# Optimization experiments

Measured on AMD Instinct MI355X. Metric: run time of the kernel, lower is better.

## Reference

```python
import jax, jax.numpy as jnp
import numpy as np

B = 1 << 20
N_FREQS = 6          # sin+cos -> 3*2*6 = 36 dims for position
N_BINS = 4           # one-blob bins -> 4 dims per scalar
W_SCALE = 0.18       # ~ sqrt(2/64) He init for ReLU


def freq_embed(p):
    # p: [B,3] -> [B, 3*2*N_FREQS] NeRF-style sin/cos frequency encoding
    freqs = (2.0 ** jnp.arange(N_FREQS, dtype=p.dtype)) * jnp.pi  # [F]
    ang = p[:, :, None] * freqs  # [B,3,F]
    return jnp.concatenate([jnp.sin(ang), jnp.cos(ang)], axis=-1).reshape(p.shape[0], -1)


def one_blob_embed(x):
    # x: [B,D] values in [0,1] -> [B, D*N_BINS] Gaussian one-blob encoding
    centers = (jnp.arange(N_BINS, dtype=x.dtype) + 0.5) / N_BINS  # [K]
    sigma = 1.0 / N_BINS
    val = jnp.exp(-0.5 * ((x[:, :, None] - centers) / sigma) ** 2)  # [B,D,K]
    return val.reshape(x.shape[0], -1)


def to_sphe_coords(d):
    # unit direction [B,3] -> normalized (theta, phi) in [0,1]^2
    theta = jnp.arccos(jnp.clip(d[:, 2], -1.0, 1.0)) / jnp.pi
    phi = jnp.arctan2(d[:, 1], d[:, 0]) / (2.0 * jnp.pi) + 0.5
    return jnp.stack([theta, phi], axis=-1)


def setup_inputs() -> dict:
    key = jax.random.key(0)
    ks = jax.random.split(key, 13)
    p = jax.random.normal(ks[0], (B, 3), dtype=jnp.float32)
    wi = jax.random.normal(ks[1], (B, 3), dtype=jnp.float32)
    wi = wi / jnp.linalg.norm(wi, axis=-1, keepdims=True)
    n = jax.random.normal(ks[2], (B, 3), dtype=jnp.float32)
    n = n / jnp.linalg.norm(n, axis=-1, keepdims=True)
    alpha = jax.random.uniform(ks[3], (B, 3), dtype=jnp.float32)
    beta = jax.random.uniform(ks[4], (B, 3), dtype=jnp.float32)
    r = jax.random.uniform(ks[5], (B, 1), dtype=jnp.float32)
    Ws = {}
    for i in range(6):
        Ws[f"W{i}"] = jax.random.normal(ks[6 + i], (64, 64), dtype=jnp.float32) * W_SCALE
    Ws["W6"] = jax.random.normal(ks[12], (3, 64), dtype=jnp.float32) * W_SCALE
    return dict(p=p, wi=wi, n=n, alpha=alpha, beta=beta, r=r, **Ws)


def reference(p, wi, n, alpha, beta, r, W0, W1, W2, W3, W4, W5, W6):
    x = jnp.concatenate([
        freq_embed(p),                               # 36
        one_blob_embed(to_sphe_coords(wi)),          # 8
        one_blob_embed(to_sphe_coords(n)),           # 8
        one_blob_embed(1.0 - jnp.exp(-r)),           # 4
        alpha,                                       # 3
        beta,                                        # 3
        jnp.ones_like(p[:, :2]),                     # 2 (implicit bias)
    ], axis=-1)  # [B,64]
    h = x
    for W in (W0, W1, W2, W3, W4, W5):
        h = jax.nn.relu(h @ W.T)
    out = h @ W6.T  # [B,3]
    return out * (alpha + beta)  # reflectance factorization
```

## Files before the change

### kernel.cpp

```cpp
#include <hip/hip_runtime.h>

typedef __attribute__((ext_vector_type(8))) short short8;
typedef __attribute__((ext_vector_type(4))) float f32x4;

typedef __attribute__((address_space(3))) unsigned short lds_us;
typedef const __attribute__((address_space(1))) unsigned short glb_us;

__device__ __forceinline__ unsigned short f2bf(float x) {
  union { float f; unsigned u; } v; v.f = x;
  unsigned r = v.u + 0x7fffu + ((v.u >> 16) & 1u);
  return (unsigned short)(r >> 16);
}

#if __has_builtin(__builtin_amdgcn_cvt_pk_bf16_f32)
__device__ __forceinline__ unsigned pk2(float a, float b) {
  return __builtin_bit_cast(unsigned, __builtin_amdgcn_cvt_pk_bf16_f32(a, b));
}
#else
__device__ __forceinline__ unsigned pk2(float a, float b) {
  union { float f; unsigned u; } x, y; x.f = a; y.f = b;
  return __builtin_amdgcn_perm(y.u + 0x8000u, x.u + 0x8000u, 0x07060302u);
}
#endif

__device__ __forceinline__ short8 u2s8(uint4 u) {
  union { uint4 a; short8 b; } c; c.a = u; return c.b;
}

__device__ __forceinline__ void wave_mem_fence() {
  asm volatile("" ::: "memory");
  __builtin_amdgcn_wave_barrier();
  asm volatile("" ::: "memory");
}

__device__ __forceinline__ void gload16(const unsigned short* g, unsigned short* l) {
  __builtin_amdgcn_global_load_lds((glb_us*)g, (lds_us*)l, 16, 0, 0);
}

__device__ __forceinline__ float acos01(float z) {
  float ax = fminf(fabsf(z), 1.0f);
  float t  = __builtin_amdgcn_sqrtf(1.0f - ax);
  float p  = fmaf(ax, fmaf(ax, fmaf(ax, -0.00596110f, 0.02363618f),
                           -0.06751692f), 0.49998766f);
  p *= t;
  return z >= 0.0f ? p : 1.0f - p;
}

__device__ __forceinline__ float atan2_01(float y, float x) {
  float ax = fabsf(x), ay = fabsf(y);
  float hi = fmaxf(ax, ay), lo = fminf(ax, ay);
  float r  = lo * __builtin_amdgcn_rcpf(fmaxf(hi, 1e-30f));
  float r2 = r * r;
  float p  = fmaf(r2, fmaf(r2, fmaf(r2, fmaf(r2, fmaf(r2,
               -0.0018655370f, 0.0083800422f), -0.018531250f),
                0.030803547f), -0.052940457f), 0.159151323f);
  float q  = r * p;
  q = (ay > ax) ? 0.25f - q : q;
  q = (x < 0.0f) ? 0.5f - q : q;
  return 0.5f + ((y >= 0.0f) ? q : -q);
}

__device__ __forceinline__ uint2 blob4pk(float x) {
  float x4 = x * 4.0f;
  float e0, e1, e2, e3;
  { float t = x4 - 0.5f; e0 = __builtin_amdgcn_exp2f(t * t * -0.72134752f); }
  { float t = x4 - 1.5f; e1 = __builtin_amdgcn_exp2f(t * t * -0.72134752f); }
  { float t = x4 - 2.5f; e2 = __builtin_amdgcn_exp2f(t * t * -0.72134752f); }
  { float t = x4 - 3.5f; e3 = __builtin_amdgcn_exp2f(t * t * -0.72134752f); }
  return make_uint2(pk2(e0, e1), pk2(e2, e3));
}

__global__ void prep_weights(
    const float* __restrict__ W0, const float* __restrict__ W1,
    const float* __restrict__ W2, const float* __restrict__ W3,
    const float* __restrict__ W4, const float* __restrict__ W5,
    const float* __restrict__ W6, unsigned short* __restrict__ wb)
{
  int idx = blockIdx.x * blockDim.x + threadIdx.x;
  if (idx < 24576) {
    int l = idx >> 12;
    const float* W = (l==0)?W0:(l==1)?W1:(l==2)?W2:(l==3)?W3:(l==4)?W4:W5;
    int j   = idx & 7;
    int ln  = (idx >> 3) & 63;
    int h   = (idx >> 9) & 1;
    int t   = (idx >> 10) & 3;
    int n15 = ln & 15, q = ln >> 4;
    int src = 32*(t>>1) + 8*(n15>>2) + 4*(t&1) + (n15&3);
    int col = h*32 + q*8 + j;
    wb[idx] = f2bf(W[src*64 + col]);
  } else if (idx < 25600) {
    int i6  = idx - 24576;
    int j   = i6 & 7;
    int ln  = (i6 >> 3) & 63;
    int h   = (i6 >> 9) & 1;
    int n15 = ln & 15, q = ln >> 4;
    wb[idx] = (n15 < 3) ? f2bf(W6[n15*64 + h*32 + q*8 + j]) : (unsigned short)0;
  }
}

__global__ __launch_bounds__(256, 3) void nrc_mlp(
    const float* __restrict__ P, const float* __restrict__ WI,
    const float* __restrict__ NRM, const float* __restrict__ ALPHA,
    const float* __restrict__ BETA, const float* __restrict__ R,
    const unsigned short* __restrict__ wb, float* __restrict__ out)
{
  __shared__ __align__(16) unsigned short Wlds[8192];
  __shared__ __align__(16) unsigned short xlds[4][64][72];
  const int lane = threadIdx.x & 63;
  const int wv   = threadIdx.x >> 6;
  unsigned short (* __restrict__ X)[72] = xlds[wv];
  const int n15 = lane & 15;
  const int q   = lane >> 4;
  const int row0 = (blockIdx.x * 4 + wv) * 64;
  const int l16 = lane * 8;

  {
    int c0 = 2*wv*512;
    gload16(wb + c0 + l16,        Wlds + c0 + l16);
    gload16(wb + c0 + 512 + l16,  Wlds + c0 + 512 + l16);
  }

  {
    const int row = row0 + lane;
    unsigned short* xr = &X[lane][0];

    float s0[6], c0[6], s1[6], c1[6], s2[6], c2[6];
    {
      float rev = 0.5f * P[row*3+0];
#pragma unroll
      for (int i = 0; i < 6; ++i) {
        float fr = __builtin_amdgcn_fractf(rev);
        s0[i] = __builtin_amdgcn_sinf(fr);
        c0[i] = __builtin_amdgcn_cosf(fr);
        rev = rev + rev;
      }
      rev = 0.5f * P[row*3+1];
#pragma unroll
      for (int i = 0; i < 6; ++i) {
        float fr = __builtin_amdgcn_fractf(rev);
        s1[i] = __builtin_amdgcn_sinf(fr);
        c1[i] = __builtin_amdgcn_cosf(fr);
        rev = rev + rev;
      }
      rev = 0.5f * P[row*3+2];
#pragma unroll
      for (int i = 0; i < 6; ++i) {
        float fr = __builtin_amdgcn_fractf(rev);
        s2[i] = __builtin_amdgcn_sinf(fr);
        c2[i] = __builtin_amdgcn_cosf(fr);
        rev = rev + rev;
      }
    }
    *(uint4*)(xr +  0) = make_uint4(pk2(s0[0],s0[1]), pk2(s0[2],s0[3]),
                                    pk2(s0[4],s0[5]), pk2(c0[0],c0[1]));
    *(uint4*)(xr +  8) = make_uint4(pk2(c0[2],c0[3]), pk2(c0[4],c0[5]),
                                    pk2(s1[0],s1[1]), pk2(s1[2],s1[3]));
    *(uint4*)(xr + 16) = make_uint4(pk2(s1[4],s1[5]), pk2(c1[0],c1[1]),
                                    pk2(c1[2],c1[3]), pk2(c1[4],c1[5]));
    *(uint4*)(xr + 24) = make_uint4(pk2(s2[0],s2[1]), pk2(s2[2],s2[3]),
                                    pk2(s2[4],s2[5]), pk2(c2[0],c2[1]));

    uint2 bwt, bwp, bnt, bnp, brr;
    {
      float wx = WI[row*3+0], wy = WI[row*3+1], wz = WI[row*3+2];
      bwt = blob4pk(acos01(wz));
      bwp = blob4pk(atan2_01(wy, wx));
    }
    {
      float nx = NRM[row*3+0], ny = NRM[row*3+1], nz = NRM[row*3+2];
      bnt = blob4pk(acos01(nz));
      bnp = blob4pk(atan2_01(ny, nx));
    }
    brr = blob4pk(1.0f - __builtin_amdgcn_exp2f(R[row] * -1.44269504f));

    *(uint4*)(xr + 32) = make_uint4(pk2(c2[2],c2[3]), pk2(c2[4],c2[5]),
                                    bwt.x, bwt.y);
    *(uint4*)(xr + 40) = make_uint4(bwp.x, bwp.y, bnt.x, bnt.y);
    *(uint4*)(xr + 48) = make_uint4(bnp.x, bnp.y, brr.x, brr.y);

    float a0 = ALPHA[row*3+0], a1 = ALPHA[row*3+1], a2 = ALPHA[row*3+2];
    float e0 = BETA[row*3+0],  e1 = BETA[row*3+1],  e2 = BETA[row*3+2];
    *(uint4*)(xr + 56) = make_uint4(pk2(a0,a1), pk2(a2,e0), pk2(e1,e2),
                                    0x3F803F80u);
  }
  wave_mem_fence();

  uint4 b0[4], b1[4];
#pragma unroll
  for (int g = 0; g < 4; ++g) {
    b0[g] = *(const uint4*)(&X[g*16 + n15][q*8]);
    b1[g] = *(const uint4*)(&X[g*16 + n15][32 + q*8]);
  }

  __syncthreads();

  const f32x4 z = {0.f, 0.f, 0.f, 0.f};

#pragma unroll
  for (int l = 0; l < 6; ++l) {
    if (l < 5) {
      int nb = ((l+1) & 1) * 4096;
      int ns = (l+1) * 4096;
      int c0 = 2*wv*512;
      gload16(wb + ns + c0 + l16,       Wlds + nb + c0 + l16);
      gload16(wb + ns + c0 + 512 + l16, Wlds + nb + c0 + 512 + l16);
    } else {
      if (wv < 2) {
        int c0 = wv*512;
        gload16(wb + 24576 + c0 + l16, Wlds + c0 + l16);
      }
    }

    const unsigned short* Wb = Wlds + (l & 1) * 4096;
    short8 a0[4], a1[4];
#pragma unroll
    for (int t = 0; t < 4; ++t) {
      a0[t] = *(const short8*)(Wb + t*1024 + l16);
      a1[t] = *(const short8*)(Wb + t*1024 + 512 + l16);
    }
#pragma unroll
    for (int g = 0; g < 4; ++g) {
      short8 bb0 = u2s8(b0[g]);
      short8 bb1 = u2s8(b1[g]);
      f32x4 acc[4];
#pragma unroll
      for (int t = 0; t < 4; ++t) {
        f32x4 c = __builtin_amdgcn_mfma_f32_16x16x32_bf16(a0[t], bb0, z, 0, 0, 0);
        acc[t]  = __builtin_amdgcn_mfma_f32_16x16x32_bf16(a1[t], bb1, c, 0, 0, 0);
      }
      uint4 n0, n1;
      n0.x = pk2(fmaxf(acc[0][0],0.f), fmaxf(acc[0][1],0.f));
      n0.y = pk2(fmaxf(acc[0][2],0.f), fmaxf(acc[0][3],0.f));
      n0.z = pk2(fmaxf(acc[1][0],0.f), fmaxf(acc[1][1],0.f));
      n0.w = pk2(fmaxf(acc[1][2],0.f), fmaxf(acc[1][3],0.f));
      n1.x = pk2(fmaxf(acc[2][0],0.f), fmaxf(acc[2][1],0.f));
      n1.y = pk2(fmaxf(acc[2][2],0.f), fmaxf(acc[2][3],0.f));
      n1.z = pk2(fmaxf(acc[3][0],0.f), fmaxf(acc[3][1],0.f));
      n1.w = pk2(fmaxf(acc[3][2],0.f), fmaxf(acc[3][3],0.f));
      b0[g] = n0; b1[g] = n1;
    }
    __syncthreads();
  }

  {
    short8 o0 = *(const short8*)(Wlds + l16);
    short8 o1 = *(const short8*)(Wlds + 512 + l16);
#pragma unroll
    for (int g = 0; g < 4; ++g) {
      f32x4 c = __builtin_amdgcn_mfma_f32_16x16x32_bf16(o0, u2s8(b0[g]), z, 0, 0, 0);
      c       = __builtin_amdgcn_mfma_f32_16x16x32_bf16(o1, u2s8(b1[g]), c, 0, 0, 0);
      if (q == 0) {
        int base = row0*3 + g*48 + n15*3;
        float3 av = *(const float3*)(ALPHA + base);
        float3 bv = *(const float3*)(BETA + base);
        float3 o;
        o.x = c[0] * (av.x + bv.x);
        o.y = c[1] * (av.y + bv.y);
        o.z = c[2] * (av.z + bv.z);
        *(float3*)(out + base) = o;
      }
    }
  }
}

extern "C" void kernel_launch(void* const* d_in, const int* in_sizes, int n_in,
                              void* d_out, int out_size, void* d_ws, size_t ws_size,
                              hipStream_t stream) {
  const float* P  = (const float*)d_in[0];
  const float* WI = (const float*)d_in[1];
  const float* NR = (const float*)d_in[2];
  const float* AL = (const float*)d_in[3];
  const float* BE = (const float*)d_in[4];
  const float* R  = (const float*)d_in[5];
  const float* W0 = (const float*)d_in[6];
  const float* W1 = (const float*)d_in[7];
  const float* W2 = (const float*)d_in[8];
  const float* W3 = (const float*)d_in[9];
  const float* W4 = (const float*)d_in[10];
  const float* W5 = (const float*)d_in[11];
  const float* W6 = (const float*)d_in[12];
  unsigned short* wb = (unsigned short*)d_ws;
  float* out = (float*)d_out;

  prep_weights<<<100, 256, 0, stream>>>(W0, W1, W2, W3, W4, W5, W6, wb);
  nrc_mlp<<<4096, 256, 0, stream>>>(P, WI, NR, AL, BE, R, wb, out);
}
```

Measured before the change: 181.5 us.

## Single-buffer weights, XOR-swizzle activation LDS, raise occupancy to 4 blocks

The double-buffered weight tile becomes a single buffer. Each layer's weights are read into registers, the block synchronises, and only then is the next layer prefetched into the same buffer. The padded 72-wide activation staging is replaced by an unpadded 64-wide layout with an XOR swizzle to avoid bank conflicts. Together these cut LDS per block so launch bounds can ask for 4 blocks per CU instead of 3. The cost is an extra barrier per layer and less overlap between the weight prefetch and the register loads.

Result: faster. 175.6 us (-3.2%).

```diff
diff --git a/kernel.cpp b/kernel.cpp
--- a/kernel.cpp
+++ b/kernel.cpp
@@ -98,17 +98,17 @@
   }
 }
 
-__global__ __launch_bounds__(256, 3) void nrc_mlp(
+__global__ __launch_bounds__(256, 4) void nrc_mlp(
     const float* __restrict__ P, const float* __restrict__ WI,
     const float* __restrict__ NRM, const float* __restrict__ ALPHA,
     const float* __restrict__ BETA, const float* __restrict__ R,
     const unsigned short* __restrict__ wb, float* __restrict__ out)
 {
-  __shared__ __align__(16) unsigned short Wlds[8192];
-  __shared__ __align__(16) unsigned short xlds[4][64][72];
+  __shared__ __align__(16) unsigned short lds[20480];
+  unsigned short* Wb = lds;
   const int lane = threadIdx.x & 63;
   const int wv   = threadIdx.x >> 6;
-  unsigned short (* __restrict__ X)[72] = xlds[wv];
+  unsigned short* Xw = lds + 4096 + (wv << 12);
   const int n15 = lane & 15;
   const int q   = lane >> 4;
   const int row0 = (blockIdx.x * 4 + wv) * 64;
@@ -116,13 +116,15 @@
 
   {
     int c0 = 2*wv*512;
-    gload16(wb + c0 + l16,        Wlds + c0 + l16);
-    gload16(wb + c0 + 512 + l16,  Wlds + c0 + 512 + l16);
+    gload16(wb + c0 + l16,        Wb + c0 + l16);
+    gload16(wb + c0 + 512 + l16,  Wb + c0 + 512 + l16);
   }
 
   {
     const int row = row0 + lane;
-    unsigned short* xr = &X[lane][0];
+    const int sw  = lane & 7;
+    unsigned short* xr = Xw + (lane << 6);
+#define XST(j) (*(uint4*)(xr + (((j) ^ sw) << 3)))
 
     float s0[6], c0[6], s1[6], c1[6], s2[6], c2[6];
     {
@@ -151,14 +153,14 @@
         rev = rev + rev;
       }
     }
-    *(uint4*)(xr +  0) = make_uint4(pk2(s0[0],s0[1]), pk2(s0[2],s0[3]),
-                                    pk2(s0[4],s0[5]), pk2(c0[0],c0[1]));
-    *(uint4*)(xr +  8) = make_uint4(pk2(c0[2],c0[3]), pk2(c0[4],c0[5]),
-                                    pk2(s1[0],s1[1]), pk2(s1[2],s1[3]));
-    *(uint4*)(xr + 16) = make_uint4(pk2(s1[4],s1[5]), pk2(c1[0],c1[1]),
-                                    pk2(c1[2],c1[3]), pk2(c1[4],c1[5]));
-    *(uint4*)(xr + 24) = make_uint4(pk2(s2[0],s2[1]), pk2(s2[2],s2[3]),
-                                    pk2(s2[4],s2[5]), pk2(c2[0],c2[1]));
+    XST(0) = make_uint4(pk2(s0[0],s0[1]), pk2(s0[2],s0[3]),
+                        pk2(s0[4],s0[5]), pk2(c0[0],c0[1]));
+    XST(1) = make_uint4(pk2(c0[2],c0[3]), pk2(c0[4],c0[5]),
+                        pk2(s1[0],s1[1]), pk2(s1[2],s1[3]));
+    XST(2) = make_uint4(pk2(s1[4],s1[5]), pk2(c1[0],c1[1]),
+                        pk2(c1[2],c1[3]), pk2(c1[4],c1[5]));
+    XST(3) = make_uint4(pk2(s2[0],s2[1]), pk2(s2[2],s2[3]),
+                        pk2(s2[4],s2[5]), pk2(c2[0],c2[1]));
 
     uint2 bwt, bwp, bnt, bnp, brr;
     {
@@ -173,23 +175,26 @@
     }
     brr = blob4pk(1.0f - __builtin_amdgcn_exp2f(R[row] * -1.44269504f));
 
-    *(uint4*)(xr + 32) = make_uint4(pk2(c2[2],c2[3]), pk2(c2[4],c2[5]),
-                                    bwt.x, bwt.y);
-    *(uint4*)(xr + 40) = make_uint4(bwp.x, bwp.y, bnt.x, bnt.y);
-    *(uint4*)(xr + 48) = make_uint4(bnp.x, bnp.y, brr.x, brr.y);
+    XST(4) = make_uint4(pk2(c2[2],c2[3]), pk2(c2[4],c2[5]), bwt.x, bwt.y);
+    XST(5) = make_uint4(bwp.x, bwp.y, bnt.x, bnt.y);
+    XST(6) = make_uint4(bnp.x, bnp.y, brr.x, brr.y);
 
     float a0 = ALPHA[row*3+0], a1 = ALPHA[row*3+1], a2 = ALPHA[row*3+2];
     float e0 = BETA[row*3+0],  e1 = BETA[row*3+1],  e2 = BETA[row*3+2];
-    *(uint4*)(xr + 56) = make_uint4(pk2(a0,a1), pk2(a2,e0), pk2(e1,e2),
-                                    0x3F803F80u);
+    XST(7) = make_uint4(pk2(a0,a1), pk2(a2,e0), pk2(e1,e2), 0x3F803F80u);
+#undef XST
   }
   wave_mem_fence();
 
   uint4 b0[4], b1[4];
-#pragma unroll
-  for (int g = 0; g < 4; ++g) {
-    b0[g] = *(const uint4*)(&X[g*16 + n15][q*8]);
-    b1[g] = *(const uint4*)(&X[g*16 + n15][32 + q*8]);
+  {
+    const int swr = n15 & 7;
+#pragma unroll
+    for (int g = 0; g < 4; ++g) {
+      const unsigned short* rb = Xw + ((g*16 + n15) << 6);
+      b0[g] = *(const uint4*)(rb + (((q    ) ^ swr) << 3));
+      b1[g] = *(const uint4*)(rb + (((q + 4) ^ swr) << 3));
+    }
   }
 
   __syncthreads();
@@ -198,26 +203,24 @@
 
 #pragma unroll
   for (int l = 0; l < 6; ++l) {
-    if (l < 5) {
-      int nb = ((l+1) & 1) * 4096;
-      int ns = (l+1) * 4096;
-      int c0 = 2*wv*512;
-      gload16(wb + ns + c0 + l16,       Wlds + nb + c0 + l16);
-      gload16(wb + ns + c0 + 512 + l16, Wlds + nb + c0 + 512 + l16);
-    } else {
-      if (wv < 2) {
-        int c0 = wv*512;
-        gload16(wb + 24576 + c0 + l16, Wlds + c0 + l16);
-      }
-    }
-
-    const unsigned short* Wb = Wlds + (l & 1) * 4096;
     short8 a0[4], a1[4];
 #pragma unroll
     for (int t = 0; t < 4; ++t) {
       a0[t] = *(const short8*)(Wb + t*1024 + l16);
       a1[t] = *(const short8*)(Wb + t*1024 + 512 + l16);
     }
+    __syncthreads();
+
+    if (l < 5) {
+      int ns = (l+1) * 4096;
+      int c0 = 2*wv*512;
+      gload16(wb + ns + c0 + l16,       Wb + c0 + l16);
+      gload16(wb + ns + c0 + 512 + l16, Wb + c0 + 512 + l16);
+    } else if (wv < 2) {
+      int c0 = wv*512;
+      gload16(wb + 24576 + c0 + l16, Wb + c0 + l16);
+    }
+
 #pragma unroll
     for (int g = 0; g < 4; ++g) {
       short8 bb0 = u2s8(b0[g]);
@@ -243,8 +246,8 @@
   }
 
   {
-    short8 o0 = *(const short8*)(Wlds + l16);
-    short8 o1 = *(const short8*)(Wlds + 512 + l16);
+    short8 o0 = *(const short8*)(Wb + l16);
+    short8 o1 = *(const short8*)(Wb + 512 + l16);
 #pragma unroll
     for (int g = 0; g < 4; ++g) {
       f32x4 c = __builtin_amdgcn_mfma_f32_16x16x32_bf16(o0, u2s8(b0[g]), z, 0, 0, 0);
```
